# Kernel optimization log

Measured on AMD Instinct MI355X. Metric: run time of the kernel, lower is better.

Reference implementation:

```python
import jax, jax.numpy as jnp
import numpy as np

B, S, H = 2, 2048, 2048
E, K = 8, 4
I_MOE, I_SH = 1408, 5632
NQ, NKV, DH = 16, 2, 128
EPS = 1e-5
ROPE_WL = 10000.0


def setup_inputs():
    key = jax.random.key(0)
    ks = jax.random.split(key, 18)
    f = lambda k, shp: jax.random.normal(k, shp, jnp.float32) * 0.02
    return {
        "decoder_sequence": jax.random.normal(ks[0], (B, S, H), jnp.float32),
        "ln1_scale": jnp.ones((H,), jnp.float32),
        "wq": f(ks[1], (H, NQ * DH)), "bq": f(ks[2], (NQ * DH,)),
        "wk": f(ks[3], (H, NKV * DH)), "bk": f(ks[4], (NKV * DH,)),
        "wv": f(ks[5], (H, NKV * DH)), "bv": f(ks[6], (NKV * DH,)),
        "wo": f(ks[7], (NQ * DH, H)),
        "ln2_scale": jnp.ones((H,), jnp.float32),
        "router_w": f(ks[8], (H, E)),
        "w_gate": f(ks[9], (E, H, I_MOE)),
        "w_up": f(ks[10], (E, H, I_MOE)),
        "w_down": f(ks[11], (E, I_MOE, H)),
        "sw_gate": f(ks[12], (H, I_SH)),
        "sw_up": f(ks[13], (H, I_SH)),
        "sw_down": f(ks[14], (I_SH, H)),
        "shared_gate_w": f(ks[15], (H, 1)),
    }


def _rms(x, scale):
    # QwenLayerNorm: RMSNorm in float32
    v = jnp.mean(jnp.square(x.astype(jnp.float32)), axis=-1, keepdims=True)
    return (x.astype(jnp.float32) * jax.lax.rsqrt(v + EPS) * scale).astype(x.dtype)


def _rope(x):
    # x: [B, S, heads, DH]; half-split rotary (keras-hub RotaryEmbedding)
    pos = jnp.arange(S, dtype=jnp.float32)
    inv = 1.0 / (ROPE_WL ** (jnp.arange(0, DH, 2, dtype=jnp.float32) / DH))
    ang = pos[:, None] * inv[None, :]                       # [S, DH/2]
    cos = jnp.cos(ang)[None, :, None, :]
    sin = jnp.sin(ang)[None, :, None, :]
    x1, x2 = jnp.split(x, 2, axis=-1)
    return jnp.concatenate([x1 * cos - x2 * sin, x2 * cos + x1 * sin], axis=-1)


def reference(decoder_sequence, ln1_scale, wq, bq, wk, bk, wv, bv, wo,
              ln2_scale, router_w, w_gate, w_up, w_down,
              sw_gate, sw_up, sw_down, shared_gate_w):
    x = decoder_sequence
    # --- self attention (pre-norm, causal, GQA, RoPE) ---
    h = _rms(x, ln1_scale)
    q = (h @ wq + bq).reshape(B, S, NQ, DH)
    k = (h @ wk + bk).reshape(B, S, NKV, DH)
    v = (h @ wv + bv).reshape(B, S, NKV, DH)
    q = _rope(q)
    k = _rope(k)
    rep = NQ // NKV
    k = jnp.repeat(k, rep, axis=2)
    v = jnp.repeat(v, rep, axis=2)
    scores = jnp.einsum('bqhd,bkhd->bhqk', q, k) / jnp.sqrt(jnp.float32(DH))
    causal = jnp.tril(jnp.ones((S, S), bool))
    scores = jnp.where(causal[None, None], scores, jnp.float32(-1e9))
    probs = jax.nn.softmax(scores, axis=-1)
    attn = jnp.einsum('bhqk,bkhd->bqhd', probs, v).reshape(B, S, NQ * DH)
    x = x + attn @ wo
    # --- sparse MoE block ---
    t = _rms(x, ln2_scale).reshape(B * S, H)
    router_logits = t @ router_w                             # [T, E]
    rw = jax.nn.softmax(router_logits, axis=-1)
    topw, topi = jax.lax.top_k(rw, K)
    topw = topw / jnp.sum(topw, axis=-1, keepdims=True)      # norm_topk_prob
    dense_w = jnp.zeros((B * S, E), t.dtype).at[
        jnp.arange(B * S)[:, None], topi].add(topw)          # [T, E]
    gate = jax.nn.silu(jnp.einsum('th,ehi->eti', t, w_gate))
    up = jnp.einsum('th,ehi->eti', t, w_up)
    eout = jnp.einsum('eti,eih->eth', gate * up, w_down)     # [E, T, H]
    moe = jnp.einsum('eth,te->th', eout, dense_w)
    # shared expert + sigmoid gate
    sh = (jax.nn.silu(t @ sw_gate) * (t @ sw_up)) @ sw_down
    sh = jax.nn.sigmoid(t @ shared_gate_w) * sh
    out = x + (moe + sh).reshape(B, S, H)
    return out
```

## Files before the change

### kernel.cpp

```cpp
#include <hip/hip_runtime.h>
#include <math.h>

static constexpr int BB   = 2;
static constexpr int SS   = 2048;
static constexpr int HH   = 2048;
static constexpr int TT   = BB * SS;
static constexpr int EE   = 8;
static constexpr int KSEL = 4;
static constexpr int IMOE = 1408;
static constexpr int ISH  = 5632;
static constexpr int NQ   = 16;
static constexpr int NKV  = 2;
static constexpr int DH   = 128;

typedef __attribute__((ext_vector_type(8))) short bhalf8;
typedef __attribute__((ext_vector_type(4))) float floatx4;

union U16B { uint4 u; bhalf8 s; };
__device__ __forceinline__ bhalf8 as_b8(uint4 u) { U16B x; x.u = u; return x.s; }

__device__ __forceinline__ void split_pack8(const float* f, uint4& hi, uint4& lo)
{
    unsigned h[4], lw[4];
#pragma unroll
    for (int q = 0; q < 4; ++q) {
        const float f0 = f[2 * q], f1 = f[2 * q + 1];
        const unsigned u0 = __float_as_uint(f0), u1 = __float_as_uint(f1);
        const unsigned m0 = u0 & 0xffff0000u, m1 = u1 & 0xffff0000u;
        h[q] = (u0 >> 16) | m1;
        const float l0 = f0 - __uint_as_float(m0);
        const float l1 = f1 - __uint_as_float(m1);
        lw[q] = (__float_as_uint(l0) >> 16) | (__float_as_uint(l1) & 0xffff0000u);
    }
    hi = make_uint4(h[0], h[1], h[2], h[3]);
    lo = make_uint4(lw[0], lw[1], lw[2], lw[3]);
}

__global__ __launch_bounds__(256)
void rmsnorm_k(const float* __restrict__ x, const float* __restrict__ sc,
               float* __restrict__ o)
{
    const int row = blockIdx.x;
    const float4* xr = (const float4*)(x + (size_t)row * HH);
    const float4* sr = (const float4*)sc;
    float4* orow = (float4*)(o + (size_t)row * HH);
    float ss = 0.f;
    for (int i = threadIdx.x; i < HH / 4; i += 256) {
        float4 v = xr[i];
        ss += v.x * v.x + v.y * v.y + v.z * v.z + v.w * v.w;
    }
#pragma unroll
    for (int off = 32; off > 0; off >>= 1) ss += __shfl_down(ss, off, 64);
    __shared__ float red[4];
    if ((threadIdx.x & 63) == 0) red[threadIdx.x >> 6] = ss;
    __syncthreads();
    const float tot = red[0] + red[1] + red[2] + red[3];
    const float inv = rsqrtf(tot / (float)HH + 1e-5f);
    for (int i = threadIdx.x; i < HH / 4; i += 256) {
        float4 v = xr[i]; float4 s = sr[i];
        float4 w;
        w.x = v.x * inv * s.x; w.y = v.y * inv * s.y;
        w.z = v.z * inv * s.z; w.w = v.w * inv * s.w;
        orow[i] = w;
    }
}

__global__ __launch_bounds__(256)
void zero_k(float* __restrict__ p, int n4)
{
    const int i = blockIdx.x * 256 + threadIdx.x;
    if (i < n4) ((float4*)p)[i] = make_float4(0.f, 0.f, 0.f, 0.f);
}

__global__ __launch_bounds__(256)
void splitw_k(const float* __restrict__ W, int K, int N,
              unsigned short* __restrict__ th, unsigned short* __restrict__ tl)
{
    const size_t zoff = (size_t)blockIdx.z * K * N;
    W += zoff; th += zoff; tl += zoff;
    __shared__ float tile[64][65];
    const int k0 = blockIdx.y * 64;
    const int n0 = blockIdx.x * 64;
    const int t  = threadIdx.x;
    const int c  = t & 63, rq = t >> 6;
#pragma unroll
    for (int r = 0; r < 16; ++r) {
        const int kk = r * 4 + rq;
        tile[kk][c] = W[(size_t)(k0 + kk) * N + n0 + c];
    }
    __syncthreads();
#pragma unroll
    for (int r = 0; r < 16; ++r) {
        const int nn = r * 4 + rq;
        const float v = tile[c][nn];
        const unsigned u  = __float_as_uint(v);
        const unsigned hm = u & 0xffff0000u;
        const float lo = v - __uint_as_float(hm);
        th[(size_t)(n0 + nn) * K + k0 + c] = (unsigned short)(u >> 16);
        tl[(size_t)(n0 + nn) * K + k0 + c] = (unsigned short)(__float_as_uint(lo) >> 16);
    }
}

__global__ __launch_bounds__(256)
void gemm_p_k(const float* __restrict__ A, int lda,
              const unsigned short* __restrict__ Bth,
              const unsigned short* __restrict__ Btl, int ldbt,
              float* __restrict__ C, int ldc, int K,
              const float* __restrict__ bias,
              const float* __restrict__ rowscale,
              const float* __restrict__ add1,
              const float* __restrict__ add2,
              int accumulate,
              const int* __restrict__ arow,
              const int* __restrict__ crow,
              const int* __restrict__ mlim)
{
    const int m0 = blockIdx.y * 128;
    if (mlim && m0 >= *mlim) return;

    __shared__ uint4 lds[2048];
    uint4* Ahi = lds;
    uint4* Alo = lds + 512;
    uint4* Bhi = lds + 1024;
    uint4* Blo = lds + 1536;

    const int t  = threadIdx.x;
    const int n0 = blockIdx.x * 128;

    const int sar = t >> 1;
    const int sak = (t & 1) << 4;
    const int sbc = t & 127;
    const int sbk = (t >> 7) << 4;
    int arow_eff = m0 + sar;
    if (arow) { const int r = arow[arow_eff]; arow_eff = (r < 0) ? 0 : r; }
    const float* Ap = A + (size_t)arow_eff * lda + sak;
    const unsigned short* Bph = Bth + (size_t)(n0 + sbc) * ldbt + sbk;
    const unsigned short* Bpl = Btl + (size_t)(n0 + sbc) * ldbt + sbk;
    const int aslot = ((sar >> 4) * 4 + (sak >> 3)) * 16 + (sar & 15);
    const int bslot = ((sbc >> 4) * 4 + (sbk >> 3)) * 16 + (sbc & 15);

    const int w  = t >> 6, l = t & 63;
    const int wr = w >> 1, wc = w & 1;
    const int lr = l & 15, kg = l >> 4;

    floatx4 acc[4][4];
#pragma unroll
    for (int i = 0; i < 4; ++i)
#pragma unroll
        for (int j = 0; j < 4; ++j) acc[i][j] = (floatx4){0.f, 0.f, 0.f, 0.f};

    float af[16];
    uint4 rbh0, rbh1, rbl0, rbl1;
    *(float4*)&af[0]  = *(const float4*)(Ap + 0);
    *(float4*)&af[4]  = *(const float4*)(Ap + 4);
    *(float4*)&af[8]  = *(const float4*)(Ap + 8);
    *(float4*)&af[12] = *(const float4*)(Ap + 12);
    rbh0 = *(const uint4*)(Bph);
    rbh1 = *(const uint4*)(Bph + 8);
    rbl0 = *(const uint4*)(Bpl);
    rbl1 = *(const uint4*)(Bpl + 8);

    for (int k0 = 0; k0 < K; k0 += 32) {
        __syncthreads();
        {
            uint4 h0, l0, h1, l1;
            split_pack8(&af[0], h0, l0);
            split_pack8(&af[8], h1, l1);
            Ahi[aslot] = h0; Ahi[aslot + 16] = h1;
            Alo[aslot] = l0; Alo[aslot + 16] = l1;
            Bhi[bslot] = rbh0; Bhi[bslot + 16] = rbh1;
            Blo[bslot] = rbl0; Blo[bslot + 16] = rbl1;
        }
        __syncthreads();

        if (k0 + 32 < K) {
            const int kn = k0 + 32;
            *(float4*)&af[0]  = *(const float4*)(Ap + kn + 0);
            *(float4*)&af[4]  = *(const float4*)(Ap + kn + 4);
            *(float4*)&af[8]  = *(const float4*)(Ap + kn + 8);
            *(float4*)&af[12] = *(const float4*)(Ap + kn + 12);
            rbh0 = *(const uint4*)(Bph + kn);
            rbh1 = *(const uint4*)(Bph + kn + 8);
            rbl0 = *(const uint4*)(Bpl + kn);
            rbl1 = *(const uint4*)(Bpl + kn + 8);
        }

        bhalf8 ah[4], al[4];
#pragma unroll
        for (int i = 0; i < 4; ++i) {
            const int s = ((wr * 4 + i) * 4 + kg) * 16 + lr;
            ah[i] = as_b8(Ahi[s]);
            al[i] = as_b8(Alo[s]);
        }
#pragma unroll
        for (int j = 0; j < 4; ++j) {
            const int s = ((wc * 4 + j) * 4 + kg) * 16 + lr;
            const bhalf8 bh = as_b8(Bhi[s]);
            const bhalf8 bl = as_b8(Blo[s]);
#pragma unroll
            for (int i = 0; i < 4; ++i) {
                acc[i][j] = __builtin_amdgcn_mfma_f32_16x16x32_bf16(ah[i], bl, acc[i][j], 0, 0, 0);
                acc[i][j] = __builtin_amdgcn_mfma_f32_16x16x32_bf16(al[i], bh, acc[i][j], 0, 0, 0);
                acc[i][j] = __builtin_amdgcn_mfma_f32_16x16x32_bf16(ah[i], bh, acc[i][j], 0, 0, 0);
            }
        }
    }

#pragma unroll
    for (int i = 0; i < 4; ++i) {
#pragma unroll
        for (int q = 0; q < 4; ++q) {
            const int m = m0 + (wr * 4 + i) * 16 + kg * 4 + q;
            int cm = m;
            if (crow) { cm = crow[m]; if (cm < 0) continue; }
            const float rs = rowscale ? rowscale[m] : 1.f;
#pragma unroll
            for (int j = 0; j < 4; ++j) {
                const int n = n0 + (wc * 4 + j) * 16 + lr;
                float v = acc[i][j][q];
                if (bias) v += bias[n];
                v *= rs;
                const size_t off = (size_t)cm * ldc + n;
                if (accumulate) v += C[off];
                if (add1) v += add1[off];
                if (add2) v += add2[off];
                C[off] = v;
            }
        }
    }
}

__global__ __launch_bounds__(256)
void gemm_f_k(const float* __restrict__ A, int lda,
              const float* __restrict__ Bm, int ldb,
              float* __restrict__ C, int ldc, int K,
              const float* __restrict__ bias,
              const float* __restrict__ rowscale,
              const float* __restrict__ add1,
              const float* __restrict__ add2,
              int accumulate,
              const int* __restrict__ arow,
              const int* __restrict__ crow,
              const int* __restrict__ mlim)
{
    const int m0 = blockIdx.y * 128;
    if (mlim && m0 >= *mlim) return;

    __shared__ uint4 lds[2048];
    uint4* Ahi = lds;
    uint4* Alo = lds + 512;
    uint4* Bhi = lds + 1024;
    uint4* Blo = lds + 1536;

    const int t  = threadIdx.x;
    const int n0 = blockIdx.x * 128;

    const int sar = t >> 1;
    const int sak = (t & 1) << 4;
    const int sbc = t & 127;
    const int sbk = (t >> 7) << 4;
    int arow_eff = m0 + sar;
    if (arow) { const int r = arow[arow_eff]; arow_eff = (r < 0) ? 0 : r; }
    const float* Ap = A + (size_t)arow_eff * lda + sak;
    const float* Bp = Bm + (size_t)sbk * ldb + n0 + sbc;
    const int aslot = ((sar >> 4) * 4 + (sak >> 3)) * 16 + (sar & 15);
    const int bslot = ((sbc >> 4) * 4 + (sbk >> 3)) * 16 + (sbc & 15);

    const int w  = t >> 6, l = t & 63;
    const int wr = w >> 1, wc = w & 1;
    const int lr = l & 15, kg = l >> 4;

    floatx4 acc[4][4];
#pragma unroll
    for (int i = 0; i < 4; ++i)
#pragma unroll
        for (int j = 0; j < 4; ++j) acc[i][j] = (floatx4){0.f, 0.f, 0.f, 0.f};

    float af[16], bf[16];
    *(float4*)&af[0]  = *(const float4*)(Ap + 0);
    *(float4*)&af[4]  = *(const float4*)(Ap + 4);
    *(float4*)&af[8]  = *(const float4*)(Ap + 8);
    *(float4*)&af[12] = *(const float4*)(Ap + 12);
#pragma unroll
    for (int j = 0; j < 16; ++j) bf[j] = Bp[(size_t)j * ldb];

    for (int k0 = 0; k0 < K; k0 += 32) {
        __syncthreads();
        {
            uint4 h0, l0, h1, l1;
            split_pack8(&af[0], h0, l0);
            split_pack8(&af[8], h1, l1);
            Ahi[aslot] = h0; Ahi[aslot + 16] = h1;
            Alo[aslot] = l0; Alo[aslot + 16] = l1;
            split_pack8(&bf[0], h0, l0);
            split_pack8(&bf[8], h1, l1);
            Bhi[bslot] = h0; Bhi[bslot + 16] = h1;
            Blo[bslot] = l0; Blo[bslot + 16] = l1;
        }
        __syncthreads();

        if (k0 + 32 < K) {
            const int kn = k0 + 32;
            *(float4*)&af[0]  = *(const float4*)(Ap + kn + 0);
            *(float4*)&af[4]  = *(const float4*)(Ap + kn + 4);
            *(float4*)&af[8]  = *(const float4*)(Ap + kn + 8);
            *(float4*)&af[12] = *(const float4*)(Ap + kn + 12);
#pragma unroll
            for (int j = 0; j < 16; ++j) bf[j] = Bp[(size_t)(kn + j) * ldb];
        }

        bhalf8 ah[4], al[4];
#pragma unroll
        for (int i = 0; i < 4; ++i) {
            const int s = ((wr * 4 + i) * 4 + kg) * 16 + lr;
            ah[i] = as_b8(Ahi[s]);
            al[i] = as_b8(Alo[s]);
        }
#pragma unroll
        for (int j = 0; j < 4; ++j) {
            const int s = ((wc * 4 + j) * 4 + kg) * 16 + lr;
            const bhalf8 bh = as_b8(Bhi[s]);
            const bhalf8 bl = as_b8(Blo[s]);
#pragma unroll
            for (int i = 0; i < 4; ++i) {
                acc[i][j] = __builtin_amdgcn_mfma_f32_16x16x32_bf16(ah[i], bl, acc[i][j], 0, 0, 0);
                acc[i][j] = __builtin_amdgcn_mfma_f32_16x16x32_bf16(al[i], bh, acc[i][j], 0, 0, 0);
                acc[i][j] = __builtin_amdgcn_mfma_f32_16x16x32_bf16(ah[i], bh, acc[i][j], 0, 0, 0);
            }
        }
    }

#pragma unroll
    for (int i = 0; i < 4; ++i) {
#pragma unroll
        for (int q = 0; q < 4; ++q) {
            const int m = m0 + (wr * 4 + i) * 16 + kg * 4 + q;
            int cm = m;
            if (crow) { cm = crow[m]; if (cm < 0) continue; }
            const float rs = rowscale ? rowscale[m] : 1.f;
#pragma unroll
            for (int j = 0; j < 4; ++j) {
                const int n = n0 + (wc * 4 + j) * 16 + lr;
                float v = acc[i][j][q];
                if (bias) v += bias[n];
                v *= rs;
                const size_t off = (size_t)cm * ldc + n;
                if (accumulate) v += C[off];
                if (add1) v += add1[off];
                if (add2) v += add2[off];
                C[off] = v;
            }
        }
    }
}

__global__ __launch_bounds__(256)
void rope_k(float* __restrict__ p, int nheads)
{
    const int idx = blockIdx.x * 256 + threadIdx.x;
    const int total = TT * nheads * (DH / 2);
    if (idx >= total) return;
    const int i  = idx & 63;
    const int hh = (idx >> 6) % nheads;
    const int tt = idx / (64 * nheads);
    const int s  = tt & (SS - 1);
    const float freq = expf(-(float)i * (9.210340371976184f / 64.f));
    const float ang = (float)s * freq;
    float sn, cs;
    sincosf(ang, &sn, &cs);
    float* base = p + ((size_t)tt * nheads + hh) * DH;
    const float x1 = base[i], x2 = base[i + 64];
    base[i]      = x1 * cs - x2 * sn;
    base[i + 64] = x2 * cs + x1 * sn;
}

static constexpr int QT   = 64;
static constexpr int KT   = 32;
static constexpr int QSTR = DH + 4;

__global__ __launch_bounds__(256)
void attn_k(const float* __restrict__ qb, const float* __restrict__ kb,
            const float* __restrict__ vb, float* __restrict__ ob)
{
    __shared__ float Qs[QT][QSTR];
    __shared__ float KVs[KT][QSTR];
    __shared__ float Ps[QT][KT + 1];
    __shared__ float Mrow[QT];
    __shared__ float Lrow[QT];

    const int t   = threadIdx.x;
    const int q0  = blockIdx.x * QT;
    const int hq  = blockIdx.y;
    const int bz  = blockIdx.z;
    const int kvh = hq >> 3;
    const float scl = 0.08838834764831845f;

    for (int i4 = t; i4 < QT * (DH / 4); i4 += 256) {
        const int qi = i4 >> 5, c4 = i4 & 31;
        float4 v = *((const float4*)(qb + ((size_t)(bz * SS + q0 + qi) * NQ + hq) * DH) + c4);
        v.x *= scl; v.y *= scl; v.z *= scl; v.w *= scl;
        *(float4*)&Qs[qi][c4 << 2] = v;
    }
    if (t < QT) { Mrow[t] = -1e30f; Lrow[t] = 0.f; }

    const int tr = t >> 4;
    const int tc = t & 15;
    float O[4][8] = {};

    const int nk = q0 + QT;
    for (int k0 = 0; k0 < nk; k0 += KT) {
        float4 kreg[4], vreg[4];
#pragma unroll
        for (int i = 0; i < 4; ++i) {
            const int idx4 = t + (i << 8);
            const int kj = idx4 >> 5, c4 = idx4 & 31;
            const size_t roff = ((size_t)(bz * SS + k0 + kj) * NKV + kvh) * DH + (c4 << 2);
            kreg[i] = *(const float4*)(kb + roff);
            vreg[i] = *(const float4*)(vb + roff);
        }
        __syncthreads();
#pragma unroll
        for (int i = 0; i < 4; ++i) {
            const int idx4 = t + (i << 8);
            *(float4*)&KVs[idx4 >> 5][(idx4 & 31) << 2] = kreg[i];
        }
        __syncthreads();

        float s0[4] = {}, s1[4] = {};
#pragma unroll 8
        for (int d = 0; d < DH; d += 4) {
            const float4 ka = *(const float4*)&KVs[tc][d];
            const float4 kb4 = *(const float4*)&KVs[tc + 16][d];
#pragma unroll
            for (int i = 0; i < 4; ++i) {
                const float4 qv = *(const float4*)&Qs[(tr << 2) + i][d];
                s0[i] += qv.x * ka.x + qv.y * ka.y + qv.z * ka.z + qv.w * ka.w;
                s1[i] += qv.x * kb4.x + qv.y * kb4.y + qv.z * kb4.z + qv.w * kb4.w;
            }
        }

#pragma unroll
        for (int i = 0; i < 4; ++i) {
            const int qg = q0 + (tr << 2) + i;
            const float a  = (k0 + tc      <= qg) ? s0[i] : -1e30f;
            const float bq_ = (k0 + tc + 16 <= qg) ? s1[i] : -1e30f;
            float mt = fmaxf(a, bq_);
#pragma unroll
            for (int o = 1; o < 16; o <<= 1) mt = fmaxf(mt, __shfl_xor(mt, o, 64));
            const float mold = Mrow[(tr << 2) + i];
            const float mnew = fmaxf(mold, mt);
            const float alpha = __expf(mold - mnew);
            const float p0 = __expf(a - mnew);
            const float p1 = __expf(bq_ - mnew);
            float ls = p0 + p1;
#pragma unroll
            for (int o = 1; o < 16; o <<= 1) ls += __shfl_xor(ls, o, 64);
            if (tc == 0) {
                Mrow[(tr << 2) + i] = mnew;
                Lrow[(tr << 2) + i] = alpha * Lrow[(tr << 2) + i] + ls;
            }
            Ps[(tr << 2) + i][tc]      = p0;
            Ps[(tr << 2) + i][tc + 16] = p1;
#pragma unroll
            for (int j = 0; j < 8; ++j) O[i][j] *= alpha;
        }
        __syncthreads();
#pragma unroll
        for (int i = 0; i < 4; ++i) {
            const int idx4 = t + (i << 8);
            *(float4*)&KVs[idx4 >> 5][(idx4 & 31) << 2] = vreg[i];
        }
        __syncthreads();

#pragma unroll 4
        for (int kj = 0; kj < KT; ++kj) {
            const float4 v0 = *(const float4*)&KVs[kj][tc << 2];
            const float4 v1 = *(const float4*)&KVs[kj][64 + (tc << 2)];
#pragma unroll
            for (int i = 0; i < 4; ++i) {
                const float p = Ps[(tr << 2) + i][kj];
                O[i][0] += p * v0.x; O[i][1] += p * v0.y;
                O[i][2] += p * v0.z; O[i][3] += p * v0.w;
                O[i][4] += p * v1.x; O[i][5] += p * v1.y;
                O[i][6] += p * v1.z; O[i][7] += p * v1.w;
            }
        }
    }

#pragma unroll
    for (int i = 0; i < 4; ++i) {
        const int qi = (tr << 2) + i;
        const float inv = 1.f / Lrow[qi];
        float* base = ob + ((size_t)(bz * SS + q0 + qi) * NQ + hq) * DH;
        float4 o0, o1;
        o0.x = O[i][0] * inv; o0.y = O[i][1] * inv; o0.z = O[i][2] * inv; o0.w = O[i][3] * inv;
        o1.x = O[i][4] * inv; o1.y = O[i][5] * inv; o1.z = O[i][6] * inv; o1.w = O[i][7] * inv;
        *(float4*)(base + (tc << 2)) = o0;
        *(float4*)(base + 64 + (tc << 2)) = o1;
    }
}

__global__ __launch_bounds__(256)
void router_k(const float* __restrict__ tb, const float* __restrict__ rw,
              const float* __restrict__ sgw, float* __restrict__ dw,
              float* __restrict__ gs)
{
    const int tok = blockIdx.x;
    const float* xr = tb + (size_t)tok * HH;
    float acc[EE] = {};
    float ag = 0.f;
    for (int h = threadIdx.x; h < HH; h += 256) {
        const float xv = xr[h];
        const float4 r0 = *(const float4*)(rw + (size_t)h * EE);
        const float4 r1 = *(const float4*)(rw + (size_t)h * EE + 4);
        acc[0] += xv * r0.x; acc[1] += xv * r0.y; acc[2] += xv * r0.z; acc[3] += xv * r0.w;
        acc[4] += xv * r1.x; acc[5] += xv * r1.y; acc[6] += xv * r1.z; acc[7] += xv * r1.w;
        ag += xv * sgw[h];
    }
#pragma unroll
    for (int e = 0; e < EE; ++e)
#pragma unroll
        for (int o = 32; o > 0; o >>= 1) acc[e] += __shfl_down(acc[e], o, 64);
#pragma unroll
    for (int o = 32; o > 0; o >>= 1) ag += __shfl_down(ag, o, 64);
    __shared__ float red[4][EE + 1];
    if ((threadIdx.x & 63) == 0) {
        const int w = threadIdx.x >> 6;
#pragma unroll
        for (int e = 0; e < EE; ++e) red[w][e] = acc[e];
        red[w][EE] = ag;
    }
    __syncthreads();
    if (threadIdx.x == 0) {
        float l[EE];
#pragma unroll
        for (int e = 0; e < EE; ++e) l[e] = red[0][e] + red[1][e] + red[2][e] + red[3][e];
        const float g = red[0][EE] + red[1][EE] + red[2][EE] + red[3][EE];
        gs[tok] = 1.f / (1.f + expf(-g));
        float m = l[0];
        for (int e = 1; e < EE; ++e) m = fmaxf(m, l[e]);
        float p[EE]; float sum = 0.f;
        for (int e = 0; e < EE; ++e) { p[e] = expf(l[e] - m); sum += p[e]; }
        for (int e = 0; e < EE; ++e) p[e] /= sum;
        bool used[EE] = {};
        float wsum = 0.f;
        for (int k = 0; k < KSEL; ++k) {
            int bi = 0; float bv = -1.f;
            for (int e = 0; e < EE; ++e)
                if (!used[e] && p[e] > bv) { bv = p[e]; bi = e; }
            used[bi] = true; wsum += bv;
        }
        for (int e = 0; e < EE; ++e)
            dw[(size_t)tok * EE + e] = used[e] ? p[e] / wsum : 0.f;
    }
}

__global__ void route_init_k(int* __restrict__ cnt)
{
    if (threadIdx.x < EE) cnt[threadIdx.x] = 0;
}

__global__ __launch_bounds__(256)
void route_fill_k(const float* __restrict__ dw, int* __restrict__ cnt,
                  int* __restrict__ tokidx, float* __restrict__ tokw)
{
    const int t = blockIdx.x * 256 + threadIdx.x;
    if (t >= TT) return;
#pragma unroll
    for (int e = 0; e < EE; ++e) {
        const float w = dw[(size_t)t * EE + e];
        if (w > 0.f) {
            const int pos = atomicAdd(cnt + e, 1);
            tokidx[e * TT + pos] = t;
            tokw[e * TT + pos]   = w;
        }
    }
}

__global__ void route_pad_k(const int* __restrict__ cnt, int* __restrict__ mpad,
                            int* __restrict__ tokidx)
{
    const int e = blockIdx.x;
    const int c = cnt[e];
    const int mp = (c + 127) & ~127;
    if (threadIdx.x == 0) mpad[e] = mp;
    for (int i = c + threadIdx.x; i < mp; i += 64) tokidx[e * TT + i] = -1;
}

__global__ __launch_bounds__(256)
void silu_mul_k(float* __restrict__ g, const float* __restrict__ u,
                const float* __restrict__ dw, int ecol, int icols, int n,
                const int* __restrict__ mlim)
{
    const int idx = blockIdx.x * 256 + threadIdx.x;
    if (idx >= n) return;
    if (mlim && idx >= (*mlim) * icols) return;
    const float gv = g[idx];
    const float uv = u[idx];
    float v = gv / (1.f + __expf(-gv)) * uv;
    if (dw) v *= dw[(size_t)(idx / icols) * EE + ecol];
    g[idx] = v;
}

extern "C" void kernel_launch(void* const* d_in, const int* in_sizes, int n_in,
                              void* d_out, int out_size, void* d_ws, size_t ws_size,
                              hipStream_t stream)
{
    (void)in_sizes; (void)n_in; (void)out_size;
    const float* x   = (const float*)d_in[0];
    const float* ln1 = (const float*)d_in[1];
    const float* wq  = (const float*)d_in[2];
    const float* bq  = (const float*)d_in[3];
    const float* wk  = (const float*)d_in[4];
    const float* bk  = (const float*)d_in[5];
    const float* wv  = (const float*)d_in[6];
    const float* bv  = (const float*)d_in[7];
    const float* wo  = (const float*)d_in[8];
    const float* ln2 = (const float*)d_in[9];
    const float* rww = (const float*)d_in[10];
    const float* wg  = (const float*)d_in[11];
    const float* wu  = (const float*)d_in[12];
    const float* wd  = (const float*)d_in[13];
    const float* swg = (const float*)d_in[14];
    const float* swu = (const float*)d_in[15];
    const float* swd = (const float*)d_in[16];
    const float* sgw = (const float*)d_in[17];
    float* out = (float*)d_out;

    float* ws   = (float*)d_ws;
    float* hbuf = ws;
    float* qb   = hbuf + (size_t)TT * HH;
    float* kb   = qb   + (size_t)TT * NQ * DH;
    float* vb   = kb   + (size_t)TT * NKV * DH;
    float* x1   = vb   + (size_t)TT * NKV * DH;
    float* moe  = x1   + (size_t)TT * HH;
    float* gbuf = moe  + (size_t)TT * HH;
    float* ubuf = gbuf + (size_t)TT * IMOE;
    float* dw   = ubuf + (size_t)TT * IMOE;
    float* gs   = dw   + (size_t)TT * EE;
    int*   tokidx = (int*)(gs + TT);
    float* tokw   = (float*)(tokidx + (size_t)EE * TT);
    int*   cnt    = (int*)(tokw + (size_t)EE * TT);
    int*   mpad   = cnt + EE;
    const size_t need_f32 = (size_t)((char*)(mpad + EE) - (char*)ws);
    if (ws_size < need_f32) return;

    char* pc0 = (char*)(mpad + EE);
    pc0 = (char*)(((uintptr_t)pc0 + 15) & ~(uintptr_t)15);
    unsigned short* p = (unsigned short*)pc0;
    unsigned short* wq_th = p; p += (size_t)HH * (NQ * DH);
    unsigned short* wq_tl = p; p += (size_t)HH * (NQ * DH);
    unsigned short* wk_th = p; p += (size_t)HH * (NKV * DH);
    unsigned short* wk_tl = p; p += (size_t)HH * (NKV * DH);
    unsigned short* wv_th = p; p += (size_t)HH * (NKV * DH);
    unsigned short* wv_tl = p; p += (size_t)HH * (NKV * DH);
    unsigned short* wo_th = p; p += (size_t)HH * HH;
    unsigned short* wo_tl = p; p += (size_t)HH * HH;
    unsigned short* wg_th = p; p += (size_t)EE * HH * IMOE;
    unsigned short* wg_tl = p; p += (size_t)EE * HH * IMOE;
    unsigned short* wu_th = p; p += (size_t)EE * HH * IMOE;
    unsigned short* wu_tl = p; p += (size_t)EE * HH * IMOE;
    unsigned short* wd_th = p; p += (size_t)EE * IMOE * HH;
    unsigned short* wd_tl = p; p += (size_t)EE * IMOE * HH;
    unsigned short* sg_th = p; p += (size_t)HH * ISH;
    unsigned short* sg_tl = p; p += (size_t)HH * ISH;
    unsigned short* su_th = p; p += (size_t)HH * ISH;
    unsigned short* su_tl = p; p += (size_t)HH * ISH;
    unsigned short* sd_th = p; p += (size_t)ISH * HH;
    unsigned short* sd_tl = p; p += (size_t)ISH * HH;
    const size_t need_planes = (size_t)((char*)p - (char*)ws);
    const bool planes = (ws_size >= need_planes);

    float* attnb = hbuf;
    float* tb    = qb;

    if (planes) {
        splitw_k<<<dim3((NQ * DH) / 64, HH / 64), 256, 0, stream>>>(wq, HH, NQ * DH, wq_th, wq_tl);
        splitw_k<<<dim3((NKV * DH) / 64, HH / 64), 256, 0, stream>>>(wk, HH, NKV * DH, wk_th, wk_tl);
        splitw_k<<<dim3((NKV * DH) / 64, HH / 64), 256, 0, stream>>>(wv, HH, NKV * DH, wv_th, wv_tl);
        splitw_k<<<dim3(HH / 64, HH / 64), 256, 0, stream>>>(wo, NQ * DH, HH, wo_th, wo_tl);
        splitw_k<<<dim3(IMOE / 64, HH / 64, EE), 256, 0, stream>>>(wg, HH, IMOE, wg_th, wg_tl);
        splitw_k<<<dim3(IMOE / 64, HH / 64, EE), 256, 0, stream>>>(wu, HH, IMOE, wu_th, wu_tl);
        splitw_k<<<dim3(HH / 64, IMOE / 64, EE), 256, 0, stream>>>(wd, IMOE, HH, wd_th, wd_tl);
        splitw_k<<<dim3(ISH / 64, HH / 64), 256, 0, stream>>>(swg, HH, ISH, sg_th, sg_tl);
        splitw_k<<<dim3(ISH / 64, HH / 64), 256, 0, stream>>>(swu, HH, ISH, su_th, su_tl);
        splitw_k<<<dim3(HH / 64, ISH / 64), 256, 0, stream>>>(swd, ISH, HH, sd_th, sd_tl);
    }

    rmsnorm_k<<<TT, 256, 0, stream>>>(x, ln1, hbuf);
    if (planes) {
        gemm_p_k<<<dim3((NQ * DH) / 128, TT / 128), 256, 0, stream>>>(hbuf, HH, wq_th, wq_tl, HH, qb, NQ * DH, HH, bq, nullptr, nullptr, nullptr, 0, nullptr, nullptr, nullptr);
        gemm_p_k<<<dim3((NKV * DH) / 128, TT / 128), 256, 0, stream>>>(hbuf, HH, wk_th, wk_tl, HH, kb, NKV * DH, HH, bk, nullptr, nullptr, nullptr, 0, nullptr, nullptr, nullptr);
        gemm_p_k<<<dim3((NKV * DH) / 128, TT / 128), 256, 0, stream>>>(hbuf, HH, wv_th, wv_tl, HH, vb, NKV * DH, HH, bv, nullptr, nullptr, nullptr, 0, nullptr, nullptr, nullptr);
    } else {
        gemm_f_k<<<dim3((NQ * DH) / 128, TT / 128), 256, 0, stream>>>(hbuf, HH, wq, NQ * DH, qb, NQ * DH, HH, bq, nullptr, nullptr, nullptr, 0, nullptr, nullptr, nullptr);
        gemm_f_k<<<dim3((NKV * DH) / 128, TT / 128), 256, 0, stream>>>(hbuf, HH, wk, NKV * DH, kb, NKV * DH, HH, bk, nullptr, nullptr, nullptr, 0, nullptr, nullptr, nullptr);
        gemm_f_k<<<dim3((NKV * DH) / 128, TT / 128), 256, 0, stream>>>(hbuf, HH, wv, NKV * DH, vb, NKV * DH, HH, bv, nullptr, nullptr, nullptr, 0, nullptr, nullptr, nullptr);
    }
    rope_k<<<(TT * NQ * 64 + 255) / 256, 256, 0, stream>>>(qb, NQ);
    rope_k<<<(TT * NKV * 64 + 255) / 256, 256, 0, stream>>>(kb, NKV);
    attn_k<<<dim3(SS / QT, NQ, BB), 256, 0, stream>>>(qb, kb, vb, attnb);
    if (planes)
        gemm_p_k<<<dim3(HH / 128, TT / 128), 256, 0, stream>>>(attnb, NQ * DH, wo_th, wo_tl, NQ * DH, x1, HH, NQ * DH, nullptr, nullptr, x, nullptr, 0, nullptr, nullptr, nullptr);
    else
        gemm_f_k<<<dim3(HH / 128, TT / 128), 256, 0, stream>>>(attnb, NQ * DH, wo, HH, x1, HH, NQ * DH, nullptr, nullptr, x, nullptr, 0, nullptr, nullptr, nullptr);
    rmsnorm_k<<<TT, 256, 0, stream>>>(x1, ln2, tb);
    router_k<<<TT, 256, 0, stream>>>(tb, rww, sgw, dw, gs);
    zero_k<<<(TT * HH / 4 + 255) / 256, 256, 0, stream>>>(moe, TT * HH / 4);
    route_init_k<<<1, 64, 0, stream>>>(cnt);
    route_fill_k<<<(TT + 255) / 256, 256, 0, stream>>>(dw, cnt, tokidx, tokw);
    route_pad_k<<<EE, 64, 0, stream>>>(cnt, mpad, tokidx);
    const int nmoe = TT * IMOE;
    for (int e = 0; e < EE; ++e) {
        const int*   idx = tokidx + e * TT;
        const float* twe = tokw + e * TT;
        const int*   ml  = mpad + e;
        if (planes) {
            gemm_p_k<<<dim3(IMOE / 128, TT / 128), 256, 0, stream>>>(tb, HH, wg_th + (size_t)e * HH * IMOE, wg_tl + (size_t)e * HH * IMOE, HH, gbuf, IMOE, HH, nullptr, nullptr, nullptr, nullptr, 0, idx, nullptr, ml);
            gemm_p_k<<<dim3(IMOE / 128, TT / 128), 256, 0, stream>>>(tb, HH, wu_th + (size_t)e * HH * IMOE, wu_tl + (size_t)e * HH * IMOE, HH, ubuf, IMOE, HH, nullptr, nullptr, nullptr, nullptr, 0, idx, nullptr, ml);
            silu_mul_k<<<(nmoe + 255) / 256, 256, 0, stream>>>(gbuf, ubuf, nullptr, 0, IMOE, nmoe, ml);
            gemm_p_k<<<dim3(HH / 128, TT / 128), 256, 0, stream>>>(gbuf, IMOE, wd_th + (size_t)e * IMOE * HH, wd_tl + (size_t)e * IMOE * HH, IMOE, moe, HH, IMOE, nullptr, twe, nullptr, nullptr, 1, nullptr, idx, ml);
        } else {
            const float* wge = wg + (size_t)e * HH * IMOE;
            const float* wue = wu + (size_t)e * HH * IMOE;
            const float* wde = wd + (size_t)e * IMOE * HH;
            gemm_f_k<<<dim3(IMOE / 128, TT / 128), 256, 0, stream>>>(tb, HH, wge, IMOE, gbuf, IMOE, HH, nullptr, nullptr, nullptr, nullptr, 0, idx, nullptr, ml);
            gemm_f_k<<<dim3(IMOE / 128, TT / 128), 256, 0, stream>>>(tb, HH, wue, IMOE, ubuf, IMOE, HH, nullptr, nullptr, nullptr, nullptr, 0, idx, nullptr, ml);
            silu_mul_k<<<(nmoe + 255) / 256, 256, 0, stream>>>(gbuf, ubuf, nullptr, 0, IMOE, nmoe, ml);
            gemm_f_k<<<dim3(HH / 128, TT / 128), 256, 0, stream>>>(gbuf, IMOE, wde, HH, moe, HH, IMOE, nullptr, twe, nullptr, nullptr, 1, nullptr, idx, ml);
        }
    }
    for (int c = 0; c < 4; ++c) {
        if (planes) {
            gemm_p_k<<<dim3(IMOE / 128, TT / 128), 256, 0, stream>>>(tb, HH, sg_th + (size_t)c * IMOE * HH, sg_tl + (size_t)c * IMOE * HH, HH, gbuf, IMOE, HH, nullptr, nullptr, nullptr, nullptr, 0, nullptr, nullptr, nullptr);
            gemm_p_k<<<dim3(IMOE / 128, TT / 128), 256, 0, stream>>>(tb, HH, su_th + (size_t)c * IMOE * HH, su_tl + (size_t)c * IMOE * HH, HH, ubuf, IMOE, HH, nullptr, nullptr, nullptr, nullptr, 0, nullptr, nullptr, nullptr);
            silu_mul_k<<<(nmoe + 255) / 256, 256, 0, stream>>>(gbuf, ubuf, nullptr, 0, IMOE, nmoe, nullptr);
            if (c < 3)
                gemm_p_k<<<dim3(HH / 128, TT / 128), 256, 0, stream>>>(gbuf, IMOE, sd_th + (size_t)c * IMOE, sd_tl + (size_t)c * IMOE, ISH, moe, HH, IMOE, nullptr, gs, nullptr, nullptr, 1, nullptr, nullptr, nullptr);
            else
                gemm_p_k<<<dim3(HH / 128, TT / 128), 256, 0, stream>>>(gbuf, IMOE, sd_th + (size_t)c * IMOE, sd_tl + (size_t)c * IMOE, ISH, out, HH, IMOE, nullptr, gs, moe, x1, 0, nullptr, nullptr, nullptr);
        } else {
            const float* swgc = swg + (size_t)c * IMOE;
            const float* swuc = swu + (size_t)c * IMOE;
            const float* swdc = swd + (size_t)c * IMOE * HH;
            gemm_f_k<<<dim3(IMOE / 128, TT / 128), 256, 0, stream>>>(tb, HH, swgc, ISH, gbuf, IMOE, HH, nullptr, nullptr, nullptr, nullptr, 0, nullptr, nullptr, nullptr);
            gemm_f_k<<<dim3(IMOE / 128, TT / 128), 256, 0, stream>>>(tb, HH, swuc, ISH, ubuf, IMOE, HH, nullptr, nullptr, nullptr, nullptr, 0, nullptr, nullptr, nullptr);
            silu_mul_k<<<(nmoe + 255) / 256, 256, 0, stream>>>(gbuf, ubuf, nullptr, 0, IMOE, nmoe, nullptr);
            if (c < 3)
                gemm_f_k<<<dim3(HH / 128, TT / 128), 256, 0, stream>>>(gbuf, IMOE, swdc, HH, moe, HH, IMOE, nullptr, gs, nullptr, nullptr, 1, nullptr, nullptr, nullptr);
            else
                gemm_f_k<<<dim3(HH / 128, TT / 128), 256, 0, stream>>>(gbuf, IMOE, swdc, HH, out, HH, IMOE, nullptr, gs, moe, x1, 0, nullptr, nullptr, nullptr);
        }
    }
}
```

Measured before the change: 5.905 ms.

## Rewrite attention kernel to use split-bf16 MFMA for QK and PV

Replaces the scalar FP32 flash-attention inner loops with bf16x3 (hi/lo split) MFMA 16x16x32 instructions for both the score and the P·V products. Q is kept in registers as packed hi/lo fragments, K and V tiles are split and packed into shared memory in MFMA operand layout, and the online-softmax state moves from shared memory into per-lane registers. This targets the attention FLOP cost on the matrix cores while keeping near-FP32 accuracy, at the cost of extra packing work, shared-memory transposes and three MFMAs per product.

```diff
diff --git a/kernel.cpp b/kernel.cpp
--- a/kernel.cpp
+++ b/kernel.cpp
@@ -374,129 +374,157 @@
     base[i + 64] = x2 * cs + x1 * sn;
 }
 
-static constexpr int QT   = 64;
-static constexpr int KT   = 32;
-static constexpr int QSTR = DH + 4;
-
 __global__ __launch_bounds__(256)
 void attn_k(const float* __restrict__ qb, const float* __restrict__ kb,
             const float* __restrict__ vb, float* __restrict__ ob)
 {
-    __shared__ float Qs[QT][QSTR];
-    __shared__ float KVs[KT][QSTR];
-    __shared__ float Ps[QT][KT + 1];
-    __shared__ float Mrow[QT];
-    __shared__ float Lrow[QT];
+    __shared__ uint4 ch_hi[512], ch_lo[512];
+    __shared__ uint4 ph_hi[256], ph_lo[256];
+    __shared__ float vscr[32 * 132];
+    __shared__ float pscr[64 * 33];
 
     const int t   = threadIdx.x;
-    const int q0  = blockIdx.x * QT;
+    const int q0  = blockIdx.x * 64;
     const int hq  = blockIdx.y;
     const int bz  = blockIdx.z;
     const int kvh = hq >> 3;
     const float scl = 0.08838834764831845f;
 
-    for (int i4 = t; i4 < QT * (DH / 4); i4 += 256) {
-        const int qi = i4 >> 5, c4 = i4 & 31;
-        float4 v = *((const float4*)(qb + ((size_t)(bz * SS + q0 + qi) * NQ + hq) * DH) + c4);
-        v.x *= scl; v.y *= scl; v.z *= scl; v.w *= scl;
-        *(float4*)&Qs[qi][c4 << 2] = v;
-    }
-    if (t < QT) { Mrow[t] = -1e30f; Lrow[t] = 0.f; }
-
-    const int tr = t >> 4;
-    const int tc = t & 15;
-    float O[4][8] = {};
-
-    const int nk = q0 + QT;
-    for (int k0 = 0; k0 < nk; k0 += KT) {
-        float4 kreg[4], vreg[4];
-#pragma unroll
-        for (int i = 0; i < 4; ++i) {
-            const int idx4 = t + (i << 8);
-            const int kj = idx4 >> 5, c4 = idx4 & 31;
-            const size_t roff = ((size_t)(bz * SS + k0 + kj) * NKV + kvh) * DH + (c4 << 2);
-            kreg[i] = *(const float4*)(kb + roff);
-            vreg[i] = *(const float4*)(vb + roff);
-        }
+    const int w  = t >> 6, l = t & 63;
+    const int lr = l & 15, kg = l >> 4;
+
+    uint4 qh[4], ql[4];
+    {
+        const float* qrow = qb + ((size_t)(bz * SS + q0 + w * 16 + lr) * NQ + hq) * DH;
+#pragma unroll
+        for (int ks = 0; ks < 4; ++ks) {
+            float f[8];
+            *(float4*)&f[0] = *(const float4*)(qrow + ks * 32 + kg * 8);
+            *(float4*)&f[4] = *(const float4*)(qrow + ks * 32 + kg * 8 + 4);
+#pragma unroll
+            for (int i = 0; i < 8; ++i) f[i] *= scl;
+            split_pack8(f, qh[ks], ql[ks]);
+        }
+    }
+
+    float m[4]    = {-1e30f, -1e30f, -1e30f, -1e30f};
+    float lsum[4] = {0.f, 0.f, 0.f, 0.f};
+    floatx4 accO[8];
+#pragma unroll
+    for (int fc = 0; fc < 8; ++fc) accO[fc] = (floatx4){0.f, 0.f, 0.f, 0.f};
+
+    const int nk = q0 + 64;
+    for (int k0 = 0; k0 < nk; k0 += 32) {
         __syncthreads();
 #pragma unroll
-        for (int i = 0; i < 4; ++i) {
-            const int idx4 = t + (i << 8);
-            *(float4*)&KVs[idx4 >> 5][(idx4 & 31) << 2] = kreg[i];
+        for (int rr = 0; rr < 2; ++rr) {
+            const int r = t + rr * 256;
+            const int ktrow = r >> 4, ri = r & 15;
+            const float* kro = kb + ((size_t)(bz * SS + k0 + ktrow) * NKV + kvh) * DH + ri * 8;
+            float f[8];
+            *(float4*)&f[0] = *(const float4*)(kro);
+            *(float4*)&f[4] = *(const float4*)(kro + 4);
+            uint4 h, lo;
+            split_pack8(f, h, lo);
+            const int slot = (((ri >> 2) * 2 + (ktrow >> 4)) * 4 + (ri & 3)) * 16 + (ktrow & 15);
+            ch_hi[slot] = h; ch_lo[slot] = lo;
+        }
+#pragma unroll
+        for (int ff = 0; ff < 4; ++ff) {
+            const int fi = t + ff * 256;
+            const int vrow = fi >> 5, c4 = fi & 31;
+            const float4 v = *(const float4*)(vb + ((size_t)(bz * SS + k0 + vrow) * NKV + kvh) * DH + c4 * 4);
+            *(float4*)&vscr[vrow * 132 + c4 * 4] = v;
         }
         __syncthreads();
 
-        float s0[4] = {}, s1[4] = {};
-#pragma unroll 8
-        for (int d = 0; d < DH; d += 4) {
-            const float4 ka = *(const float4*)&KVs[tc][d];
-            const float4 kb4 = *(const float4*)&KVs[tc + 16][d];
-#pragma unroll
-            for (int i = 0; i < 4; ++i) {
-                const float4 qv = *(const float4*)&Qs[(tr << 2) + i][d];
-                s0[i] += qv.x * ka.x + qv.y * ka.y + qv.z * ka.z + qv.w * ka.w;
-                s1[i] += qv.x * kb4.x + qv.y * kb4.y + qv.z * kb4.z + qv.w * kb4.w;
+        floatx4 sa[2];
+        sa[0] = (floatx4){0.f, 0.f, 0.f, 0.f};
+        sa[1] = (floatx4){0.f, 0.f, 0.f, 0.f};
+#pragma unroll
+        for (int ks = 0; ks < 4; ++ks) {
+#pragma unroll
+            for (int j = 0; j < 2; ++j) {
+                const int s = ((ks * 2 + j) * 4 + kg) * 16 + lr;
+                const bhalf8 kh = as_b8(ch_hi[s]);
+                const bhalf8 kl = as_b8(ch_lo[s]);
+                const bhalf8 aqh = as_b8(qh[ks]);
+                const bhalf8 aql = as_b8(ql[ks]);
+                sa[j] = __builtin_amdgcn_mfma_f32_16x16x32_bf16(aqh, kl, sa[j], 0, 0, 0);
+                sa[j] = __builtin_amdgcn_mfma_f32_16x16x32_bf16(aql, kh, sa[j], 0, 0, 0);
+                sa[j] = __builtin_amdgcn_mfma_f32_16x16x32_bf16(aqh, kh, sa[j], 0, 0, 0);
             }
         }
 
-#pragma unroll
-        for (int i = 0; i < 4; ++i) {
-            const int qg = q0 + (tr << 2) + i;
-            const float a  = (k0 + tc      <= qg) ? s0[i] : -1e30f;
-            const float bq_ = (k0 + tc + 16 <= qg) ? s1[i] : -1e30f;
-            float mt = fmaxf(a, bq_);
+        float alpha[4];
+#pragma unroll
+        for (int q = 0; q < 4; ++q) {
+            const int rowg = q0 + w * 16 + kg * 4 + q;
+            float s0 = sa[0][q], s1 = sa[1][q];
+            if (k0 + lr > rowg)      s0 = -1e30f;
+            if (k0 + 16 + lr > rowg) s1 = -1e30f;
+            float mt = fmaxf(s0, s1);
 #pragma unroll
             for (int o = 1; o < 16; o <<= 1) mt = fmaxf(mt, __shfl_xor(mt, o, 64));
-            const float mold = Mrow[(tr << 2) + i];
-            const float mnew = fmaxf(mold, mt);
-            const float alpha = __expf(mold - mnew);
-            const float p0 = __expf(a - mnew);
-            const float p1 = __expf(bq_ - mnew);
+            const float mnew = fmaxf(m[q], mt);
+            alpha[q] = __expf(m[q] - mnew);
+            const float p0 = __expf(s0 - mnew);
+            const float p1 = __expf(s1 - mnew);
             float ls = p0 + p1;
 #pragma unroll
             for (int o = 1; o < 16; o <<= 1) ls += __shfl_xor(ls, o, 64);
-            if (tc == 0) {
-                Mrow[(tr << 2) + i] = mnew;
-                Lrow[(tr << 2) + i] = alpha * Lrow[(tr << 2) + i] + ls;
-            }
-            Ps[(tr << 2) + i][tc]      = p0;
-            Ps[(tr << 2) + i][tc + 16] = p1;
-#pragma unroll
-            for (int j = 0; j < 8; ++j) O[i][j] *= alpha;
+            m[q] = mnew;
+            lsum[q] = alpha[q] * lsum[q] + ls;
+            const int row_local = w * 16 + kg * 4 + q;
+            pscr[row_local * 33 + lr]      = p0;
+            pscr[row_local * 33 + 16 + lr] = p1;
+#pragma unroll
+            for (int fc = 0; fc < 8; ++fc) accO[fc][q] *= alpha[q];
         }
         __syncthreads();
-#pragma unroll
-        for (int i = 0; i < 4; ++i) {
-            const int idx4 = t + (i << 8);
-            *(float4*)&KVs[idx4 >> 5][(idx4 & 31) << 2] = vreg[i];
+
+        {
+            const int plr = t & 15, pkg = (t >> 4) & 3, prb = t >> 6;
+            float f[8];
+#pragma unroll
+            for (int i = 0; i < 8; ++i) f[i] = pscr[(prb * 16 + plr) * 33 + pkg * 8 + i];
+            uint4 h, lo;
+            split_pack8(f, h, lo);
+            ph_hi[t] = h; ph_lo[t] = lo;
+        }
+#pragma unroll
+        for (int rr = 0; rr < 2; ++rr) {
+            const int s = t + rr * 256;
+            const int vlr = s & 15, vkg = (s >> 4) & 3, vfc = s >> 6;
+            float g[8];
+#pragma unroll
+            for (int i = 0; i < 8; ++i) g[i] = vscr[(vkg * 8 + i) * 132 + vfc * 16 + vlr];
+            uint4 vh, vl;
+            split_pack8(g, vh, vl);
+            ch_hi[s] = vh; ch_lo[s] = vl;
         }
         __syncthreads();
 
-#pragma unroll 4
-        for (int kj = 0; kj < KT; ++kj) {
-            const float4 v0 = *(const float4*)&KVs[kj][tc << 2];
-            const float4 v1 = *(const float4*)&KVs[kj][64 + (tc << 2)];
-#pragma unroll
-            for (int i = 0; i < 4; ++i) {
-                const float p = Ps[(tr << 2) + i][kj];
-                O[i][0] += p * v0.x; O[i][1] += p * v0.y;
-                O[i][2] += p * v0.z; O[i][3] += p * v0.w;
-                O[i][4] += p * v1.x; O[i][5] += p * v1.y;
-                O[i][6] += p * v1.z; O[i][7] += p * v1.w;
-            }
-        }
-    }
-
-#pragma unroll
-    for (int i = 0; i < 4; ++i) {
-        const int qi = (tr << 2) + i;
-        const float inv = 1.f / Lrow[qi];
-        float* base = ob + ((size_t)(bz * SS + q0 + qi) * NQ + hq) * DH;
-        float4 o0, o1;
-        o0.x = O[i][0] * inv; o0.y = O[i][1] * inv; o0.z = O[i][2] * inv; o0.w = O[i][3] * inv;
-        o1.x = O[i][4] * inv; o1.y = O[i][5] * inv; o1.z = O[i][6] * inv; o1.w = O[i][7] * inv;
-        *(float4*)(base + (tc << 2)) = o0;
-        *(float4*)(base + 64 + (tc << 2)) = o1;
+        const bhalf8 pah = as_b8(ph_hi[(w * 4 + kg) * 16 + lr]);
+        const bhalf8 pal = as_b8(ph_lo[(w * 4 + kg) * 16 + lr]);
+#pragma unroll
+        for (int fc = 0; fc < 8; ++fc) {
+            const int s = (fc * 4 + kg) * 16 + lr;
+            const bhalf8 vh = as_b8(ch_hi[s]);
+            const bhalf8 vl = as_b8(ch_lo[s]);
+            accO[fc] = __builtin_amdgcn_mfma_f32_16x16x32_bf16(pah, vl, accO[fc], 0, 0, 0);
+            accO[fc] = __builtin_amdgcn_mfma_f32_16x16x32_bf16(pal, vh, accO[fc], 0, 0, 0);
+            accO[fc] = __builtin_amdgcn_mfma_f32_16x16x32_bf16(pah, vh, accO[fc], 0, 0, 0);
+        }
+    }
+
+#pragma unroll
+    for (int q = 0; q < 4; ++q) {
+        const float inv = 1.f / lsum[q];
+        float* orow = ob + ((size_t)(bz * SS + q0 + w * 16 + kg * 4 + q) * NQ + hq) * DH;
+#pragma unroll
+        for (int fc = 0; fc < 8; ++fc)
+            orow[fc * 16 + lr] = accO[fc][q] * inv;
     }
 }
 
@@ -699,7 +727,7 @@
     }
     rope_k<<<(TT * NQ * 64 + 255) / 256, 256, 0, stream>>>(qb, NQ);
     rope_k<<<(TT * NKV * 64 + 255) / 256, 256, 0, stream>>>(kb, NKV);
-    attn_k<<<dim3(SS / QT, NQ, BB), 256, 0, stream>>>(qb, kb, vb, attnb);
+    attn_k<<<dim3(SS / 64, NQ, BB), 256, 0, stream>>>(qb, kb, vb, attnb);
     if (planes)
         gemm_p_k<<<dim3(HH / 128, TT / 128), 256, 0, stream>>>(attnb, NQ * DH, wo_th, wo_tl, NQ * DH, x1, HH, NQ * DH, nullptr, nullptr, x, nullptr, 0, nullptr, nullptr, nullptr);
     else
```

Result: faster. 4.861 ms (-17.7%).
